# Performance work log

Measured on AMD Instinct MI355X. Metric: run time of the kernel, lower is better.

The kernel has to match this reference:

```python
import jax, jax.numpy as jnp
import numpy as np

DEPTH = 3

def _rx(theta):
    c, s = jnp.cos(theta / 2), jnp.sin(theta / 2)
    return jnp.stack([jnp.stack([c + 0j, -1j * s], -1),
                      jnp.stack([-1j * s, c + 0j], -1)], -2)

def _ry(theta):
    c, s = jnp.cos(theta / 2), jnp.sin(theta / 2)
    return jnp.stack([jnp.stack([c + 0j, -s + 0j], -1),
                      jnp.stack([s + 0j, c + 0j], -1)], -2)

def _rz(theta):
    e = jnp.exp(-0.5j * theta.astype(jnp.complex64))
    z = jnp.zeros_like(e)
    return jnp.stack([jnp.stack([e, z], -1),
                      jnp.stack([z, jnp.conj(e)], -1)], -2)

def _apply_1q(state, U, q):
    # state: (batch, 2,2,...,2); wire q lives on axis q+1. U: (2,2) or (batch,2,2)
    s = jnp.moveaxis(state, q + 1, -1)
    if U.ndim == 3:
        s = jnp.einsum('b...i,bji->b...j', s, U)
    else:
        s = jnp.einsum('...i,ji->...j', s, U)
    return jnp.moveaxis(s, -1, q + 1)

def _apply_cnot(state, c, t):
    s = jnp.moveaxis(state, (c + 1, t + 1), (-2, -1))
    s = jnp.concatenate([s[..., 0:1, :], s[..., 1:2, ::-1]], axis=-2)
    return jnp.moveaxis(s, (-2, -1), (c + 1, t + 1))

def _circuit(x, params):
    batch, n = x.shape
    depth = params.shape[0]
    state = jnp.zeros((batch,) + (2,) * n, jnp.complex64)
    state = state.at[(slice(None),) + (0,) * n].set(1.0)
    # data-encoding RX with per-sample angles
    for q in range(n):
        state = _apply_1q(state, _rx(x[:, q].astype(jnp.complex64).real), q)
    for l in range(depth):
        for q in range(n):
            state = _apply_1q(state, _rx(params[l, q, 0]), q)
            state = _apply_1q(state, _ry(params[l, q, 1]), q)
            state = _apply_1q(state, _rz(params[l, q, 2]), q)
        for q in range(n - 1):
            state = _apply_cnot(state, q, q + 1)
        state = _apply_cnot(state, n - 1, 0)
    probs = state.real ** 2 + state.imag ** 2  # (batch, 2,...,2)
    exps = []
    for w in range(n):
        p = jnp.moveaxis(probs, w + 1, 1).reshape(batch, 2, -1).sum(-1)
        exps.append(p[:, 0] - p[:, 1])  # <Z_w> = P(0) - P(1)
    return jnp.stack(exps, axis=1)


def setup_inputs() -> dict:
    key = jax.random.key(0)
    k1, k2 = jax.random.split(key)
    batch, n = 128, 14
    x = jax.random.normal(k1, (batch, n), dtype=jnp.float32)
    params = jax.random.normal(k2, (DEPTH, n, 3), dtype=jnp.float32)
    return {"x": x, "params": params}


def reference(x, params):
    return _circuit(x, params)
```

## Files before the change

kernel.cpp:

```cpp
#include <hip/hip_runtime.h>

namespace {

using v2f = __attribute__((ext_vector_type(2))) float;

constexpr int NQ      = 14;
constexpr int NSTATES = 1 << NQ;
constexpr int BLOCK   = 1024;
constexpr int NWAVES  = BLOCK / 64;

constexpr unsigned cparity(unsigned x){ x^=x>>8; x^=x>>4; x^=x>>2; x^=x>>1; return x&1u; }

struct Mat { unsigned row[NQ]; unsigned col[NQ]; };

constexpr Mat m_after(int nr){
  Mat m{};
  for(int p=0;p<NQ;++p){ m.row[p]=1u<<p; m.col[p]=1u<<p; }
  for(int l=0;l<nr;++l)
    for(int q=0;q<NQ;++q){
      int cq=(q==NQ-1)?NQ-1:q, tq=(q==NQ-1)?0:q+1;
      int Pc=NQ-1-cq, Pt=NQ-1-tq;
      m.row[Pt]^=m.row[Pc]; m.col[Pc]^=m.col[Pt];
    }
  return m;
}

constexpr Mat M1=m_after(1), M2=m_after(2), M3=m_after(3);
constexpr unsigned amask(int q){ return M1.col[NQ-1-q]; }
constexpr unsigned arow (int q){ return M1.row[NQ-1-q]; }
constexpr unsigned bmask(int q){ return M2.col[NQ-1-q]; }
constexpr unsigned brow (int q){ return M2.row[NQ-1-q]; }

constexpr int rank_of(const unsigned* v, int n){
  unsigned a[24]{};
  for(int i=0;i<n;++i) a[i]=v[i];
  int r=0;
  for(int bit=15;bit>=0;--bit){
    int p=-1;
    for(int i=r;i<n;++i){ if((a[i]>>bit)&1){ p=i; break; } }
    if(p<0) continue;
    unsigned t=a[r]; a[r]=a[p]; a[p]=t;
    for(int i=0;i<n;++i) if(i!=r && ((a[i]>>bit)&1)) a[i]^=a[r];
    ++r;
  }
  return r;
}

struct Plan {
  unsigned A[14], B[14], C[14];
  int BlaneGi[6]; unsigned BlanePi4[6];
  int BregGi[4];  unsigned BregEps[4];
  int CregGi[4];  unsigned CregEps[4];
  int ClaneGi[4]; unsigned ClaneEps[4];
  unsigned EJ4[14], ET[14];
};

constexpr Plan make_plan(){
  Plan P{};
  for(int t=0;t<14;++t) P.A[t]=amask(t);
  for(int t=0;t<4;++t){ P.B[t]=amask(10+t); P.BregGi[t]=10+t; }
  bool used[14]{}; int picked[14]{}; int np=0;
  {
    unsigned cur[20]{}; int nc=0;
    for(int t=0;t<4;++t) cur[nc++]=P.B[t];
    for(int q=0;q<14 && np<10;++q){
      cur[nc]=bmask(q);
      if(rank_of(cur,nc+1)==nc+1){ ++nc; picked[np++]=q; used[q]=true; }
    }
  }
  for(int i=0;i<6;++i){ P.B[4+i]=bmask(picked[i]); P.BlaneGi[i]=14+picked[i]; }
  int wq[4]{}, un[4]{}; int nu=0;
  for(int i=0;i<4;++i){ wq[i]=picked[6+i]; P.B[10+i]=bmask(wq[i]); P.CregGi[i]=14+wq[i]; }
  for(int q=0;q<14;++q) if(!used[q]) un[nu++]=q;
  for(int i=0;i<4;++i) P.ClaneGi[i]=14+un[i];
  for(int i=0;i<4;++i){ unsigned m=0;
    for(int t=0;t<10;++t) m |= cparity(arow(10+i)&P.B[4+t])<<t;
    P.BregEps[i]=m; }
  for(int i=0;i<6;++i){ unsigned m=0;
    for(int t=0;t<4;++t) m |= cparity(brow(picked[i])&P.B[t])<<t;
    P.BlanePi4[i]=m; }
  for(int t=0;t<4;++t) P.C[t]=bmask(wq[t]);
  for(int t=0;t<4;++t) P.C[4+t]=bmask(un[t]);
  {
    unsigned cc[20]{}; int n=0;
    for(int t=0;t<8;++t) cc[n++]=P.C[t];
    int pos=8;
    for(int p=0;p<14 && pos<14;++p){
      cc[n]=1u<<p;
      if(rank_of(cc,n+1)==n+1){ P.C[pos]=1u<<p; ++n; ++pos; }
    }
  }
  for(int i=0;i<4;++i){ unsigned m=0;
    for(int t=0;t<10;++t) m |= cparity(brow(wq[i])&P.C[4+t])<<t;
    P.CregEps[i]=m; }
  for(int i=0;i<4;++i){ unsigned m=0;
    for(int t=0;t<10;++t){ if(t==i) continue; m |= cparity(brow(un[i])&P.C[4+t])<<t; }
    P.ClaneEps[i]=m; }
  for(int w=0;w<14;++w){
    unsigned R=M3.row[NQ-1-w]; unsigned mj=0, mt=0;
    for(int t=0;t<4;++t)  mj |= cparity(R&P.C[t])<<t;
    for(int t=0;t<10;++t) mt |= cparity(R&P.C[4+t])<<t;
    P.EJ4[w]=mj; P.ET[w]=mt;
  }
  return P;
}

constexpr Plan PL = make_plan();
static_assert(rank_of(PL.A,14)==14, "phase A map not bijective");
static_assert(rank_of(PL.B,14)==14, "phase B map not bijective");
static_assert(rank_of(PL.C,14)==14, "phase C map not bijective");

struct Inv { unsigned col[NQ]; };
constexpr Inv inv_basis(const unsigned* bas){
  unsigned vec[NQ]{}, cmb[NQ]{}; bool used[NQ]{}; int pivk[NQ]{};
  for(int k=0;k<NQ;++k){ vec[k]=bas[k]; cmb[k]=1u<<k; }
  for(int b=0;b<NQ;++b){
    int p=-1;
    for(int k=0;k<NQ;++k) if(!used[k] && ((vec[k]>>b)&1)){ p=k; break; }
    used[p]=true; pivk[b]=p;
    for(int k=0;k<NQ;++k) if(k!=p && ((vec[k]>>b)&1)){ vec[k]^=vec[p]; cmb[k]^=cmb[p]; }
  }
  Inv R{};
  for(int b=0;b<NQ;++b) R.col[b]=cmb[pivk[b]];
  return R;
}
constexpr bool check_inv(const unsigned* bas, const Inv& iv){
  for(int p=0;p<NQ;++p){
    unsigned s=0;
    for(int k=0;k<NQ;++k) if((iv.col[p]>>k)&1) s^=bas[k];
    if(s != (1u<<p)) return false;
  }
  return true;
}
constexpr Inv IA = inv_basis(PL.A), IB = inv_basis(PL.B), IC = inv_basis(PL.C);
static_assert(check_inv(PL.A, IA), "IA");
static_assert(check_inv(PL.B, IB), "IB");
static_assert(check_inv(PL.C, IC), "IC");

struct Trans { unsigned t[NQ]; };
constexpr Trans trans_phys(const Inv& iv){
  Trans T{};
  for(int p=0;p<NQ;++p) T.t[p]=iv.col[p];
  return T;
}
constexpr Trans trans_of(const unsigned* cur, const Inv& iv){
  Trans T{};
  for(int k=0;k<NQ;++k){
    unsigned c=0;
    for(int p=0;p<NQ;++p) if((cur[k]>>p)&1) c^=iv.col[p];
    T.t[k]=c;
  }
  return T;
}
constexpr Trans T_PA = trans_phys(IA);
constexpr Trans T_AB = trans_of(PL.A, IB);
constexpr Trans T_BC = trans_of(PL.B, IC);

struct CJ { unsigned v[16]; };
constexpr CJ mk_cj(const Trans& T){
  CJ c{};
  for(int j=0;j<16;++j){
    unsigned s=0;
    for(int b=0;b<4;++b) if((j>>b)&1) s^=T.t[b];
    c.v[j]=s;
  }
  return c;
}
constexpr CJ CJ_PA=mk_cj(T_PA), CJ_AB=mk_cj(T_AB), CJ_BC=mk_cj(T_BC);

__device__ __forceinline__ v2f mkv(float a, float b){ v2f r; r[0]=a; r[1]=b; return r; }

__device__ __forceinline__ v2f pk_mul(v2f a, v2f b){
  v2f d; asm("v_pk_mul_f32 %0, %1, %2 op_sel:[0,0] op_sel_hi:[1,1]" : "=v"(d) : "v"(a), "v"(b)); return d;
}
__device__ __forceinline__ v2f pk_fma(v2f a, v2f b, v2f c){
  v2f d; asm("v_pk_fma_f32 %0, %1, %2, %3 op_sel:[0,0,0] op_sel_hi:[1,1,1]" : "=v"(d) : "v"(a), "v"(b), "v"(c)); return d;
}
__device__ __forceinline__ v2f pk_fma_swap1(v2f a, v2f b, v2f c){
  v2f d; asm("v_pk_fma_f32 %0, %1, %2, %3 op_sel:[0,1,0] op_sel_hi:[1,0,1]" : "=v"(d) : "v"(a), "v"(b), "v"(c)); return d;
}
__device__ __forceinline__ v2f cmul_pk(v2f uxx, v2f uyn, v2f s){ return pk_fma_swap1(uyn, s, pk_mul(uxx, s)); }
__device__ __forceinline__ v2f cfma_pk(v2f uxx, v2f uyn, v2f s, v2f acc){ return pk_fma_swap1(uyn, s, pk_fma(uxx, s, acc)); }

__device__ __forceinline__ float2 cmulf(float2 a, float2 b){
  return make_float2(a.x*b.x - a.y*b.y, a.x*b.y + a.y*b.x);
}
__device__ __forceinline__ v2f sel2(bool c, v2f x, v2f y){ v2f r; r[0]=c?x[0]:y[0]; r[1]=c?x[1]:y[1]; return r; }

struct GC { v2f u00x,u00n,u01x,u01n,u10x,u10n,u11x,u11n; };
__device__ __forceinline__ GC load_gc(const v2f* __restrict__ g){
  GC c{g[0],g[1],g[2],g[3],g[4],g[5],g[6],g[7]}; return c;
}

template<int CTRL>
__device__ __forceinline__ int dpp(int x){
  return __builtin_amdgcn_update_dpp(0, x, CTRL, 0xF, 0xF, true);
}
__device__ __forceinline__ int x32(int x, unsigned lane){
  auto r = __builtin_amdgcn_permlane32_swap((unsigned)x, (unsigned)x, false, false);
  return (lane & 32u) ? (int)r[0] : (int)r[1];
}
template<int K>
__device__ __forceinline__ v2f xpart(v2f v, unsigned lane){
  int x0=__float_as_int(v[0]), x1=__float_as_int(v[1]);
  int y0, y1;
  if constexpr (K==0){ y0=dpp<0xB1>(x0);  y1=dpp<0xB1>(x1); }
  else if constexpr (K==1){ y0=dpp<0x4E>(x0);  y1=dpp<0x4E>(x1); }
  else if constexpr (K==2){
    y0=__builtin_amdgcn_ds_swizzle(x0,0x101F);
    y1=__builtin_amdgcn_ds_swizzle(x1,0x101F);
  }
  else if constexpr (K==3){ y0=dpp<0x128>(x0); y1=dpp<0x128>(x1); }
  else if constexpr (K==4){
    y0=__builtin_amdgcn_ds_swizzle(x0,0x401F);
    y1=__builtin_amdgcn_ds_swizzle(x1,0x401F);
  }
  else { y0=x32(x0,lane); y1=x32(x1,lane); }
  v2f r; r[0]=__int_as_float(y0); r[1]=__int_as_float(y1); return r;
}

template<int BIT>
__device__ __forceinline__ void reg_gate(v2f (&a)[16], const GC& c, bool eps){
  v2f m00x=sel2(eps,c.u11x,c.u00x), m00n=sel2(eps,c.u11n,c.u00n);
  v2f m01x=sel2(eps,c.u10x,c.u01x), m01n=sel2(eps,c.u10n,c.u01n);
  v2f m10x=sel2(eps,c.u01x,c.u10x), m10n=sel2(eps,c.u01n,c.u10n);
  v2f m11x=sel2(eps,c.u00x,c.u11x), m11n=sel2(eps,c.u00n,c.u11n);
#pragma unroll
  for(int v=0; v<16; ++v){
    if(!((v>>BIT)&1)){
      int w = v | (1<<BIT);
      v2f a0=a[v], a1=a[w];
      a[v] = cfma_pk(m01x,m01n,a1, cmul_pk(m00x,m00n,a0));
      a[w] = cfma_pk(m11x,m11n,a1, cmul_pk(m10x,m10n,a0));
    }
  }
}

template<int XK, unsigned PI4>
__device__ __forceinline__ void lane_gate(v2f (&a)[16], const GC& c, bool sel, unsigned lane){
  v2f kax0=sel2(sel,c.u11x,c.u00x), kan0=sel2(sel,c.u11n,c.u00n);
  v2f kbx0=sel2(sel,c.u10x,c.u01x), kbn0=sel2(sel,c.u10n,c.u01n);
  v2f kax1=sel2(sel,c.u00x,c.u11x), kan1=sel2(sel,c.u00n,c.u11n);
  v2f kbx1=sel2(sel,c.u01x,c.u10x), kbn1=sel2(sel,c.u01n,c.u10n);
#pragma unroll
  for(int j=0;j<16;++j){
    v2f th = xpart<XK>(a[j], lane);
    bool pi = (__builtin_popcount(PI4 & (unsigned)j) & 1) != 0;
    v2f kax = pi?kax1:kax0, kan = pi?kan1:kan0;
    v2f kbx = pi?kbx1:kbx0, kbn = pi?kbn1:kbn0;
    a[j] = cfma_pk(kbx,kbn,th, cmul_pk(kax,kan,a[j]));
  }
}

__device__ __forceinline__ unsigned nb_of(unsigned tid, const unsigned (&t)[NQ]){
  unsigned s=0;
#pragma unroll
  for(int k=0;k<10;++k) s ^= t[4+k] & (0u-((tid>>k)&1u));
  return s;
}

__device__ __forceinline__ void scatter16(v2f* __restrict__ st, const v2f (&a)[16],
                                          unsigned nb, const CJ& cj){
#pragma unroll
  for(int j=0;j<16;++j){
    unsigned d = nb ^ cj.v[j];
    st[d + (d>>4)] = a[j];
  }
}

__global__ void prep_gates(const float* __restrict__ prm, float* __restrict__ wsf){
  int t = threadIdx.x;
  if(t >= 2*NQ) return;
  int l = 1 + t/NQ, q = t % NQ;
  float ax=prm[(l*NQ+q)*3+0], ay=prm[(l*NQ+q)*3+1], az=prm[(l*NQ+q)*3+2];
  float cx,sx,cy,sy,cz,sz;
  sincosf(0.5f*ax,&sx,&cx); sincosf(0.5f*ay,&sy,&cy); sincosf(0.5f*az,&sz,&cz);
  float2 M00=make_float2(cy*cx, sy*sx),  M01=make_float2(-sy*cx,-cy*sx);
  float2 M10=make_float2(sy*cx,-cy*sx),  M11=make_float2(cy*cx,-sy*sx);
  float2 ez =make_float2(cz,-sz), ezc=make_float2(cz,sz);
  float2 U00=cmulf(ez,M00), U01=cmulf(ez,M01), U10=cmulf(ezc,M10), U11=cmulf(ezc,M11);
  float* o = wsf + t*16;
  o[0]=U00.x; o[1]=U00.x; o[2]=-U00.y; o[3]=U00.y;
  o[4]=U01.x; o[5]=U01.x; o[6]=-U01.y; o[7]=U01.y;
  o[8]=U10.x; o[9]=U10.x; o[10]=-U10.y; o[11]=U10.y;
  o[12]=U11.x; o[13]=U11.x; o[14]=-U11.y; o[15]=U11.y;
}

__global__ __launch_bounds__(BLOCK, 4) void qsim_kernel(
    const float* __restrict__ x,
    const float* __restrict__ prm,
    const float* __restrict__ gw,
    float* __restrict__ out)
{
  __shared__ v2f    st[BLOCK*17];
  __shared__ v2f    Utab[28*8];
  __shared__ float2 l0c[NQ][2];
  __shared__ float  red[NWAVES][NQ];

  const int b = blockIdx.x;
  const unsigned tid = threadIdx.x;
  const unsigned lane = tid & 63u;

  if(tid < 28*16) ((float*)Utab)[tid] = gw[tid];
  if(tid < NQ){
    int q = tid;
    float ax = prm[q*3+0] + x[b*NQ+q];
    float ay = prm[q*3+1], az = prm[q*3+2];
    float cx,sx,cy,sy,cz,sz;
    sincosf(0.5f*ax,&sx,&cx); sincosf(0.5f*ay,&sy,&cy); sincosf(0.5f*az,&sz,&cz);
    l0c[q][0] = cmulf(make_float2(cz,-sz), make_float2(cy*cx,  sy*sx));
    l0c[q][1] = cmulf(make_float2(cz, sz), make_float2(sy*cx, -cy*sx));
  }
  __syncthreads();

  {
    float2 Pk = l0c[0][(tid>>9)&1];
#pragma unroll
    for(int q=1;q<10;++q) Pk = cmulf(Pk, l0c[q][(tid>>(9-q))&1]);
    float2 t2[2], t4[4];
    t2[0]=cmulf(Pk,l0c[10][0]); t2[1]=cmulf(Pk,l0c[10][1]);
#pragma unroll
    for(int i=0;i<2;++i){ t4[2*i]=cmulf(t2[i],l0c[11][0]); t4[2*i+1]=cmulf(t2[i],l0c[11][1]); }
    v2f a[16];
#pragma unroll
    for(int j=0;j<16;++j){
      float2 v = cmulf(cmulf(t4[j>>2], l0c[12][(j>>1)&1]), l0c[13][j&1]);
      a[j] = mkv(v.x, v.y);
    }
    scatter16(st, a, nb_of(tid, T_PA.t), CJ_PA);
  }
  __syncthreads();

  {
    v2f a[16];
    const int rb = (int)tid*17;
#pragma unroll
    for(int j=0;j<16;++j) a[j] = st[rb + j];
    reg_gate<0>(a, load_gc(Utab+0*8), false);
    reg_gate<1>(a, load_gc(Utab+1*8), false);
    reg_gate<2>(a, load_gc(Utab+2*8), false);
    reg_gate<3>(a, load_gc(Utab+3*8), false);
    lane_gate<0,0u>(a, load_gc(Utab+4*8), (tid&1)!=0,  lane);
    lane_gate<1,0u>(a, load_gc(Utab+5*8), (tid&2)!=0,  lane);
    lane_gate<2,0u>(a, load_gc(Utab+6*8), (tid&4)!=0,  lane);
    lane_gate<3,0u>(a, load_gc(Utab+7*8), (tid&8)!=0,  lane);
    lane_gate<4,0u>(a, load_gc(Utab+8*8), (tid&16)!=0, lane);
    lane_gate<5,0u>(a, load_gc(Utab+9*8), (tid&32)!=0, lane);
    __syncthreads();
    scatter16(st, a, nb_of(tid, T_AB.t), CJ_AB);
  }
  __syncthreads();

  {
    v2f a[16];
    const int rb = (int)tid*17;
#pragma unroll
    for(int j=0;j<16;++j) a[j] = st[rb + j];
    reg_gate<0>(a, load_gc(Utab+PL.BregGi[0]*8), (__builtin_popcount(PL.BregEps[0]&tid)&1)!=0);
    reg_gate<1>(a, load_gc(Utab+PL.BregGi[1]*8), (__builtin_popcount(PL.BregEps[1]&tid)&1)!=0);
    reg_gate<2>(a, load_gc(Utab+PL.BregGi[2]*8), (__builtin_popcount(PL.BregEps[2]&tid)&1)!=0);
    reg_gate<3>(a, load_gc(Utab+PL.BregGi[3]*8), (__builtin_popcount(PL.BregEps[3]&tid)&1)!=0);
    lane_gate<0,PL.BlanePi4[0]>(a, load_gc(Utab+PL.BlaneGi[0]*8), (tid&1)!=0,  lane);
    lane_gate<1,PL.BlanePi4[1]>(a, load_gc(Utab+PL.BlaneGi[1]*8), (tid&2)!=0,  lane);
    lane_gate<2,PL.BlanePi4[2]>(a, load_gc(Utab+PL.BlaneGi[2]*8), (tid&4)!=0,  lane);
    lane_gate<3,PL.BlanePi4[3]>(a, load_gc(Utab+PL.BlaneGi[3]*8), (tid&8)!=0,  lane);
    lane_gate<4,PL.BlanePi4[4]>(a, load_gc(Utab+PL.BlaneGi[4]*8), (tid&16)!=0, lane);
    lane_gate<5,PL.BlanePi4[5]>(a, load_gc(Utab+PL.BlaneGi[5]*8), (tid&32)!=0, lane);
    __syncthreads();
    scatter16(st, a, nb_of(tid, T_BC.t), CJ_BC);
  }
  __syncthreads();

  {
    v2f a[16];
    const int rb = (int)tid*17;
#pragma unroll
    for(int j=0;j<16;++j) a[j] = st[rb + j];
    reg_gate<0>(a, load_gc(Utab+PL.CregGi[0]*8), (__builtin_popcount(PL.CregEps[0]&tid)&1)!=0);
    reg_gate<1>(a, load_gc(Utab+PL.CregGi[1]*8), (__builtin_popcount(PL.CregEps[1]&tid)&1)!=0);
    reg_gate<2>(a, load_gc(Utab+PL.CregGi[2]*8), (__builtin_popcount(PL.CregEps[2]&tid)&1)!=0);
    reg_gate<3>(a, load_gc(Utab+PL.CregGi[3]*8), (__builtin_popcount(PL.CregEps[3]&tid)&1)!=0);
    lane_gate<0,0u>(a, load_gc(Utab+PL.ClaneGi[0]*8),
        (((tid&1u)!=0) != ((__builtin_popcount(PL.ClaneEps[0]&tid)&1)!=0)), lane);
    lane_gate<1,0u>(a, load_gc(Utab+PL.ClaneGi[1]*8),
        (((tid&2u)!=0) != ((__builtin_popcount(PL.ClaneEps[1]&tid)&1)!=0)), lane);
    lane_gate<2,0u>(a, load_gc(Utab+PL.ClaneGi[2]*8),
        (((tid&4u)!=0) != ((__builtin_popcount(PL.ClaneEps[2]&tid)&1)!=0)), lane);
    lane_gate<3,0u>(a, load_gc(Utab+PL.ClaneGi[3]*8),
        (((tid&8u)!=0) != ((__builtin_popcount(PL.ClaneEps[3]&tid)&1)!=0)), lane);

    float acc[NQ];
#pragma unroll
    for(int w=0;w<NQ;++w) acc[w]=0.f;
#pragma unroll
    for(int j=0;j<16;++j){
      float p = a[j][0]*a[j][0] + a[j][1]*a[j][1];
#pragma unroll
      for(int w=0;w<NQ;++w){
        if(__builtin_popcount(PL.EJ4[w] & (unsigned)j) & 1) acc[w]-=p; else acc[w]+=p;
      }
    }
    const int wave = tid >> 6;
#pragma unroll
    for(int w=0;w<NQ;++w){
      float v = (__builtin_popcount(PL.ET[w]&tid)&1) ? -acc[w] : acc[w];
#pragma unroll
      for(int off=32; off>0; off>>=1) v += __shfl_down(v, off, 64);
      if(lane==0) red[wave][w]=v;
    }
    __syncthreads();
    if(tid < NQ){
      float s=0.f;
#pragma unroll
      for(int wv=0; wv<NWAVES; ++wv) s += red[wv][tid];
      out[b*NQ + tid] = s;
    }
  }
}

}

extern "C" void kernel_launch(void* const* d_in, const int* in_sizes, int n_in,
                              void* d_out, int out_size, void* d_ws, size_t ws_size,
                              hipStream_t stream) {
  const float* x   = (const float*)d_in[0];
  const float* prm = (const float*)d_in[1];
  float* out = (float*)d_out;
  const int batch = in_sizes[0] / NQ;
  prep_gates<<<1, 64, 0, stream>>>(prm, (float*)d_ws);
  qsim_kernel<<<batch, BLOCK, 0, stream>>>(x, prm, (const float*)d_ws, out);
}
```

Before: 43.67 us.

## Fuse gate prep into main kernel, drop packed-FP asm, use Walsh-Hadamard reduction

After: 37.97 us. 13.1% less time.

```diff
diff --git a/kernel.cpp b/kernel.cpp
--- a/kernel.cpp
+++ b/kernel.cpp
@@ -1,8 +1,6 @@
 #include <hip/hip_runtime.h>
 
 namespace {
-
-using v2f = __attribute__((ext_vector_type(2))) float;
 
 constexpr int NQ      = 14;
 constexpr int NSTATES = 1 << NQ;
@@ -168,28 +166,26 @@
 }
 constexpr CJ CJ_PA=mk_cj(T_PA), CJ_AB=mk_cj(T_AB), CJ_BC=mk_cj(T_BC);
 
-__device__ __forceinline__ v2f mkv(float a, float b){ v2f r; r[0]=a; r[1]=b; return r; }
-
-__device__ __forceinline__ v2f pk_mul(v2f a, v2f b){
-  v2f d; asm("v_pk_mul_f32 %0, %1, %2 op_sel:[0,0] op_sel_hi:[1,1]" : "=v"(d) : "v"(a), "v"(b)); return d;
-}
-__device__ __forceinline__ v2f pk_fma(v2f a, v2f b, v2f c){
-  v2f d; asm("v_pk_fma_f32 %0, %1, %2, %3 op_sel:[0,0,0] op_sel_hi:[1,1,1]" : "=v"(d) : "v"(a), "v"(b), "v"(c)); return d;
-}
-__device__ __forceinline__ v2f pk_fma_swap1(v2f a, v2f b, v2f c){
-  v2f d; asm("v_pk_fma_f32 %0, %1, %2, %3 op_sel:[0,1,0] op_sel_hi:[1,0,1]" : "=v"(d) : "v"(a), "v"(b), "v"(c)); return d;
-}
-__device__ __forceinline__ v2f cmul_pk(v2f uxx, v2f uyn, v2f s){ return pk_fma_swap1(uyn, s, pk_mul(uxx, s)); }
-__device__ __forceinline__ v2f cfma_pk(v2f uxx, v2f uyn, v2f s, v2f acc){ return pk_fma_swap1(uyn, s, pk_fma(uxx, s, acc)); }
-
-__device__ __forceinline__ float2 cmulf(float2 a, float2 b){
-  return make_float2(a.x*b.x - a.y*b.y, a.x*b.y + a.y*b.x);
-}
-__device__ __forceinline__ v2f sel2(bool c, v2f x, v2f y){ v2f r; r[0]=c?x[0]:y[0]; r[1]=c?x[1]:y[1]; return r; }
-
-struct GC { v2f u00x,u00n,u01x,u01n,u10x,u10n,u11x,u11n; };
-__device__ __forceinline__ GC load_gc(const v2f* __restrict__ g){
-  GC c{g[0],g[1],g[2],g[3],g[4],g[5],g[6],g[7]}; return c;
+__device__ __forceinline__ float2 cmul2(float2 a, float2 b){
+  return make_float2(fmaf(a.x, b.x, -(a.y * b.y)),
+                     fmaf(a.x, b.y,  a.y * b.x));
+}
+__device__ __forceinline__ float2 cfma2(float2 a, float2 b, float2 c){
+  return make_float2(fmaf(a.x, b.x, fmaf(-a.y, b.y, c.x)),
+                     fmaf(a.x, b.y, fmaf( a.y, b.x, c.y)));
+}
+__device__ __forceinline__ float2 sel2f(bool c, float2 x, float2 y){
+  return make_float2(c ? x.x : y.x, c ? x.y : y.y);
+}
+
+struct GC { float2 u00,u01,u10,u11; };
+__device__ __forceinline__ GC load_gc(const float2* __restrict__ g){
+  const float4* p = reinterpret_cast<const float4*>(g);
+  float4 q0=p[0], q1=p[1];
+  GC c;
+  c.u00=make_float2(q0.x,q0.y); c.u01=make_float2(q0.z,q0.w);
+  c.u10=make_float2(q1.x,q1.y); c.u11=make_float2(q1.z,q1.w);
+  return c;
 }
 
 template<int CTRL>
@@ -201,8 +197,8 @@
   return (lane & 32u) ? (int)r[0] : (int)r[1];
 }
 template<int K>
-__device__ __forceinline__ v2f xpart(v2f v, unsigned lane){
-  int x0=__float_as_int(v[0]), x1=__float_as_int(v[1]);
+__device__ __forceinline__ float2 xpart(float2 v, unsigned lane){
+  int x0=__float_as_int(v.x), x1=__float_as_int(v.y);
   int y0, y1;
   if constexpr (K==0){ y0=dpp<0xB1>(x0);  y1=dpp<0xB1>(x1); }
   else if constexpr (K==1){ y0=dpp<0x4E>(x0);  y1=dpp<0x4E>(x1); }
@@ -216,39 +212,36 @@
     y1=__builtin_amdgcn_ds_swizzle(x1,0x401F);
   }
   else { y0=x32(x0,lane); y1=x32(x1,lane); }
-  v2f r; r[0]=__int_as_float(y0); r[1]=__int_as_float(y1); return r;
+  return make_float2(__int_as_float(y0), __int_as_float(y1));
 }
 
 template<int BIT>
-__device__ __forceinline__ void reg_gate(v2f (&a)[16], const GC& c, bool eps){
-  v2f m00x=sel2(eps,c.u11x,c.u00x), m00n=sel2(eps,c.u11n,c.u00n);
-  v2f m01x=sel2(eps,c.u10x,c.u01x), m01n=sel2(eps,c.u10n,c.u01n);
-  v2f m10x=sel2(eps,c.u01x,c.u10x), m10n=sel2(eps,c.u01n,c.u10n);
-  v2f m11x=sel2(eps,c.u00x,c.u11x), m11n=sel2(eps,c.u00n,c.u11n);
+__device__ __forceinline__ void reg_gate(float2 (&a)[16], const GC& c, bool eps){
+  float2 m00=sel2f(eps,c.u11,c.u00), m01=sel2f(eps,c.u10,c.u01);
+  float2 m10=sel2f(eps,c.u01,c.u10), m11=sel2f(eps,c.u00,c.u11);
 #pragma unroll
   for(int v=0; v<16; ++v){
     if(!((v>>BIT)&1)){
       int w = v | (1<<BIT);
-      v2f a0=a[v], a1=a[w];
-      a[v] = cfma_pk(m01x,m01n,a1, cmul_pk(m00x,m00n,a0));
-      a[w] = cfma_pk(m11x,m11n,a1, cmul_pk(m10x,m10n,a0));
+      float2 a0=a[v], a1=a[w];
+      a[v] = cfma2(m01, a1, cmul2(m00, a0));
+      a[w] = cfma2(m11, a1, cmul2(m10, a0));
     }
   }
 }
 
 template<int XK, unsigned PI4>
-__device__ __forceinline__ void lane_gate(v2f (&a)[16], const GC& c, bool sel, unsigned lane){
-  v2f kax0=sel2(sel,c.u11x,c.u00x), kan0=sel2(sel,c.u11n,c.u00n);
-  v2f kbx0=sel2(sel,c.u10x,c.u01x), kbn0=sel2(sel,c.u10n,c.u01n);
-  v2f kax1=sel2(sel,c.u00x,c.u11x), kan1=sel2(sel,c.u00n,c.u11n);
-  v2f kbx1=sel2(sel,c.u01x,c.u10x), kbn1=sel2(sel,c.u01n,c.u10n);
+__device__ __forceinline__ void lane_gate(float2 (&a)[16], const GC& c, bool sel, unsigned lane){
+  float2 ka0=sel2f(sel,c.u11,c.u00), kb0=sel2f(sel,c.u10,c.u01);
+  float2 ka1=sel2f(sel,c.u00,c.u11), kb1=sel2f(sel,c.u01,c.u10);
+  float2 th[16];
+#pragma unroll
+  for(int j=0;j<16;++j) th[j] = xpart<XK>(a[j], lane);
 #pragma unroll
   for(int j=0;j<16;++j){
-    v2f th = xpart<XK>(a[j], lane);
     bool pi = (__builtin_popcount(PI4 & (unsigned)j) & 1) != 0;
-    v2f kax = pi?kax1:kax0, kan = pi?kan1:kan0;
-    v2f kbx = pi?kbx1:kbx0, kbn = pi?kbn1:kbn0;
-    a[j] = cfma_pk(kbx,kbn,th, cmul_pk(kax,kan,a[j]));
+    float2 ka = pi?ka1:ka0, kb = pi?kb1:kb0;
+    a[j] = cfma2(kb, th[j], cmul2(ka, a[j]));
   }
 }
 
@@ -259,7 +252,7 @@
   return s;
 }
 
-__device__ __forceinline__ void scatter16(v2f* __restrict__ st, const v2f (&a)[16],
+__device__ __forceinline__ void scatter16(float2* __restrict__ st, const float2 (&a)[16],
                                           unsigned nb, const CJ& cj){
 #pragma unroll
   for(int j=0;j<16;++j){
@@ -268,32 +261,13 @@
   }
 }
 
-__global__ void prep_gates(const float* __restrict__ prm, float* __restrict__ wsf){
-  int t = threadIdx.x;
-  if(t >= 2*NQ) return;
-  int l = 1 + t/NQ, q = t % NQ;
-  float ax=prm[(l*NQ+q)*3+0], ay=prm[(l*NQ+q)*3+1], az=prm[(l*NQ+q)*3+2];
-  float cx,sx,cy,sy,cz,sz;
-  sincosf(0.5f*ax,&sx,&cx); sincosf(0.5f*ay,&sy,&cy); sincosf(0.5f*az,&sz,&cz);
-  float2 M00=make_float2(cy*cx, sy*sx),  M01=make_float2(-sy*cx,-cy*sx);
-  float2 M10=make_float2(sy*cx,-cy*sx),  M11=make_float2(cy*cx,-sy*sx);
-  float2 ez =make_float2(cz,-sz), ezc=make_float2(cz,sz);
-  float2 U00=cmulf(ez,M00), U01=cmulf(ez,M01), U10=cmulf(ezc,M10), U11=cmulf(ezc,M11);
-  float* o = wsf + t*16;
-  o[0]=U00.x; o[1]=U00.x; o[2]=-U00.y; o[3]=U00.y;
-  o[4]=U01.x; o[5]=U01.x; o[6]=-U01.y; o[7]=U01.y;
-  o[8]=U10.x; o[9]=U10.x; o[10]=-U10.y; o[11]=U10.y;
-  o[12]=U11.x; o[13]=U11.x; o[14]=-U11.y; o[15]=U11.y;
-}
-
 __global__ __launch_bounds__(BLOCK, 4) void qsim_kernel(
     const float* __restrict__ x,
     const float* __restrict__ prm,
-    const float* __restrict__ gw,
     float* __restrict__ out)
 {
-  __shared__ v2f    st[BLOCK*17];
-  __shared__ v2f    Utab[28*8];
+  __shared__ float2 st[BLOCK*17];
+  __shared__ alignas(16) float2 Utab[28*4];
   __shared__ float2 l0c[NQ][2];
   __shared__ float  red[NWAVES][NQ];
 
@@ -301,109 +275,126 @@
   const unsigned tid = threadIdx.x;
   const unsigned lane = tid & 63u;
 
-  if(tid < 28*16) ((float*)Utab)[tid] = gw[tid];
+  if(tid < 28){
+    int t = tid;
+    int l = 1 + t/NQ, q = t % NQ;
+    float ax=prm[(l*NQ+q)*3+0], ay=prm[(l*NQ+q)*3+1], az=prm[(l*NQ+q)*3+2];
+    float cx,sx,cy,sy,cz,sz;
+    sincosf(0.5f*ax,&sx,&cx); sincosf(0.5f*ay,&sy,&cy); sincosf(0.5f*az,&sz,&cz);
+    float2 M00=make_float2(cy*cx, sy*sx),  M01=make_float2(-sy*cx,-cy*sx);
+    float2 M10=make_float2(sy*cx,-cy*sx),  M11=make_float2(cy*cx,-sy*sx);
+    float2 ez =make_float2(cz,-sz), ezc=make_float2(cz,sz);
+    float2* U = &Utab[t*4];
+    U[0]=cmul2(ez,M00); U[1]=cmul2(ez,M01);
+    U[2]=cmul2(ezc,M10); U[3]=cmul2(ezc,M11);
+  }
   if(tid < NQ){
     int q = tid;
     float ax = prm[q*3+0] + x[b*NQ+q];
     float ay = prm[q*3+1], az = prm[q*3+2];
     float cx,sx,cy,sy,cz,sz;
     sincosf(0.5f*ax,&sx,&cx); sincosf(0.5f*ay,&sy,&cy); sincosf(0.5f*az,&sz,&cz);
-    l0c[q][0] = cmulf(make_float2(cz,-sz), make_float2(cy*cx,  sy*sx));
-    l0c[q][1] = cmulf(make_float2(cz, sz), make_float2(sy*cx, -cy*sx));
+    l0c[q][0] = cmul2(make_float2(cz,-sz), make_float2(cy*cx,  sy*sx));
+    l0c[q][1] = cmul2(make_float2(cz, sz), make_float2(sy*cx, -cy*sx));
   }
   __syncthreads();
 
   {
-    float2 Pk = l0c[0][(tid>>9)&1];
-#pragma unroll
-    for(int q=1;q<10;++q) Pk = cmulf(Pk, l0c[q][(tid>>(9-q))&1]);
+    float2 p01 = cmul2(l0c[0][(tid>>9)&1],  l0c[1][(tid>>8)&1]);
+    float2 p23 = cmul2(l0c[2][(tid>>7)&1],  l0c[3][(tid>>6)&1]);
+    float2 p45 = cmul2(l0c[4][(tid>>5)&1],  l0c[5][(tid>>4)&1]);
+    float2 p67 = cmul2(l0c[6][(tid>>3)&1],  l0c[7][(tid>>2)&1]);
+    float2 p89 = cmul2(l0c[8][(tid>>1)&1],  l0c[9][tid&1]);
+    float2 Pk  = cmul2(cmul2(cmul2(p01,p23), cmul2(p45,p67)), p89);
     float2 t2[2], t4[4];
-    t2[0]=cmulf(Pk,l0c[10][0]); t2[1]=cmulf(Pk,l0c[10][1]);
-#pragma unroll
-    for(int i=0;i<2;++i){ t4[2*i]=cmulf(t2[i],l0c[11][0]); t4[2*i+1]=cmulf(t2[i],l0c[11][1]); }
-    v2f a[16];
+    t2[0]=cmul2(Pk,l0c[10][0]); t2[1]=cmul2(Pk,l0c[10][1]);
+#pragma unroll
+    for(int i=0;i<2;++i){ t4[2*i]=cmul2(t2[i],l0c[11][0]); t4[2*i+1]=cmul2(t2[i],l0c[11][1]); }
+    float2 a[16];
 #pragma unroll
     for(int j=0;j<16;++j){
-      float2 v = cmulf(cmulf(t4[j>>2], l0c[12][(j>>1)&1]), l0c[13][j&1]);
-      a[j] = mkv(v.x, v.y);
+      a[j] = cmul2(cmul2(t4[j>>2], l0c[12][(j>>1)&1]), l0c[13][j&1]);
     }
     scatter16(st, a, nb_of(tid, T_PA.t), CJ_PA);
   }
   __syncthreads();
 
   {
-    v2f a[16];
+    float2 a[16];
     const int rb = (int)tid*17;
 #pragma unroll
     for(int j=0;j<16;++j) a[j] = st[rb + j];
-    reg_gate<0>(a, load_gc(Utab+0*8), false);
-    reg_gate<1>(a, load_gc(Utab+1*8), false);
-    reg_gate<2>(a, load_gc(Utab+2*8), false);
-    reg_gate<3>(a, load_gc(Utab+3*8), false);
-    lane_gate<0,0u>(a, load_gc(Utab+4*8), (tid&1)!=0,  lane);
-    lane_gate<1,0u>(a, load_gc(Utab+5*8), (tid&2)!=0,  lane);
-    lane_gate<2,0u>(a, load_gc(Utab+6*8), (tid&4)!=0,  lane);
-    lane_gate<3,0u>(a, load_gc(Utab+7*8), (tid&8)!=0,  lane);
-    lane_gate<4,0u>(a, load_gc(Utab+8*8), (tid&16)!=0, lane);
-    lane_gate<5,0u>(a, load_gc(Utab+9*8), (tid&32)!=0, lane);
+    reg_gate<0>(a, load_gc(Utab+0*4), false);
+    reg_gate<1>(a, load_gc(Utab+1*4), false);
+    reg_gate<2>(a, load_gc(Utab+2*4), false);
+    reg_gate<3>(a, load_gc(Utab+3*4), false);
+    lane_gate<0,0u>(a, load_gc(Utab+4*4), (tid&1)!=0,  lane);
+    lane_gate<1,0u>(a, load_gc(Utab+5*4), (tid&2)!=0,  lane);
+    lane_gate<2,0u>(a, load_gc(Utab+6*4), (tid&4)!=0,  lane);
+    lane_gate<3,0u>(a, load_gc(Utab+7*4), (tid&8)!=0,  lane);
+    lane_gate<4,0u>(a, load_gc(Utab+8*4), (tid&16)!=0, lane);
+    lane_gate<5,0u>(a, load_gc(Utab+9*4), (tid&32)!=0, lane);
     __syncthreads();
     scatter16(st, a, nb_of(tid, T_AB.t), CJ_AB);
   }
   __syncthreads();
 
   {
-    v2f a[16];
+    float2 a[16];
     const int rb = (int)tid*17;
 #pragma unroll
     for(int j=0;j<16;++j) a[j] = st[rb + j];
-    reg_gate<0>(a, load_gc(Utab+PL.BregGi[0]*8), (__builtin_popcount(PL.BregEps[0]&tid)&1)!=0);
-    reg_gate<1>(a, load_gc(Utab+PL.BregGi[1]*8), (__builtin_popcount(PL.BregEps[1]&tid)&1)!=0);
-    reg_gate<2>(a, load_gc(Utab+PL.BregGi[2]*8), (__builtin_popcount(PL.BregEps[2]&tid)&1)!=0);
-    reg_gate<3>(a, load_gc(Utab+PL.BregGi[3]*8), (__builtin_popcount(PL.BregEps[3]&tid)&1)!=0);
-    lane_gate<0,PL.BlanePi4[0]>(a, load_gc(Utab+PL.BlaneGi[0]*8), (tid&1)!=0,  lane);
-    lane_gate<1,PL.BlanePi4[1]>(a, load_gc(Utab+PL.BlaneGi[1]*8), (tid&2)!=0,  lane);
-    lane_gate<2,PL.BlanePi4[2]>(a, load_gc(Utab+PL.BlaneGi[2]*8), (tid&4)!=0,  lane);
-    lane_gate<3,PL.BlanePi4[3]>(a, load_gc(Utab+PL.BlaneGi[3]*8), (tid&8)!=0,  lane);
-    lane_gate<4,PL.BlanePi4[4]>(a, load_gc(Utab+PL.BlaneGi[4]*8), (tid&16)!=0, lane);
-    lane_gate<5,PL.BlanePi4[5]>(a, load_gc(Utab+PL.BlaneGi[5]*8), (tid&32)!=0, lane);
+    reg_gate<0>(a, load_gc(Utab+PL.BregGi[0]*4), (__builtin_popcount(PL.BregEps[0]&tid)&1)!=0);
+    reg_gate<1>(a, load_gc(Utab+PL.BregGi[1]*4), (__builtin_popcount(PL.BregEps[1]&tid)&1)!=0);
+    reg_gate<2>(a, load_gc(Utab+PL.BregGi[2]*4), (__builtin_popcount(PL.BregEps[2]&tid)&1)!=0);
+    reg_gate<3>(a, load_gc(Utab+PL.BregGi[3]*4), (__builtin_popcount(PL.BregEps[3]&tid)&1)!=0);
+    lane_gate<0,PL.BlanePi4[0]>(a, load_gc(Utab+PL.BlaneGi[0]*4), (tid&1)!=0,  lane);
+    lane_gate<1,PL.BlanePi4[1]>(a, load_gc(Utab+PL.BlaneGi[1]*4), (tid&2)!=0,  lane);
+    lane_gate<2,PL.BlanePi4[2]>(a, load_gc(Utab+PL.BlaneGi[2]*4), (tid&4)!=0,  lane);
+    lane_gate<3,PL.BlanePi4[3]>(a, load_gc(Utab+PL.BlaneGi[3]*4), (tid&8)!=0,  lane);
+    lane_gate<4,PL.BlanePi4[4]>(a, load_gc(Utab+PL.BlaneGi[4]*4), (tid&16)!=0, lane);
+    lane_gate<5,PL.BlanePi4[5]>(a, load_gc(Utab+PL.BlaneGi[5]*4), (tid&32)!=0, lane);
     __syncthreads();
     scatter16(st, a, nb_of(tid, T_BC.t), CJ_BC);
   }
   __syncthreads();
 
   {
-    v2f a[16];
+    float2 a[16];
     const int rb = (int)tid*17;
 #pragma unroll
     for(int j=0;j<16;++j) a[j] = st[rb + j];
-    reg_gate<0>(a, load_gc(Utab+PL.CregGi[0]*8), (__builtin_popcount(PL.CregEps[0]&tid)&1)!=0);
-    reg_gate<1>(a, load_gc(Utab+PL.CregGi[1]*8), (__builtin_popcount(PL.CregEps[1]&tid)&1)!=0);
-    reg_gate<2>(a, load_gc(Utab+PL.CregGi[2]*8), (__builtin_popcount(PL.CregEps[2]&tid)&1)!=0);
-    reg_gate<3>(a, load_gc(Utab+PL.CregGi[3]*8), (__builtin_popcount(PL.CregEps[3]&tid)&1)!=0);
-    lane_gate<0,0u>(a, load_gc(Utab+PL.ClaneGi[0]*8),
+    reg_gate<0>(a, load_gc(Utab+PL.CregGi[0]*4), (__builtin_popcount(PL.CregEps[0]&tid)&1)!=0);
+    reg_gate<1>(a, load_gc(Utab+PL.CregGi[1]*4), (__builtin_popcount(PL.CregEps[1]&tid)&1)!=0);
+    reg_gate<2>(a, load_gc(Utab+PL.CregGi[2]*4), (__builtin_popcount(PL.CregEps[2]&tid)&1)!=0);
+    reg_gate<3>(a, load_gc(Utab+PL.CregGi[3]*4), (__builtin_popcount(PL.CregEps[3]&tid)&1)!=0);
+    lane_gate<0,0u>(a, load_gc(Utab+PL.ClaneGi[0]*4),
         (((tid&1u)!=0) != ((__builtin_popcount(PL.ClaneEps[0]&tid)&1)!=0)), lane);
-    lane_gate<1,0u>(a, load_gc(Utab+PL.ClaneGi[1]*8),
+    lane_gate<1,0u>(a, load_gc(Utab+PL.ClaneGi[1]*4),
         (((tid&2u)!=0) != ((__builtin_popcount(PL.ClaneEps[1]&tid)&1)!=0)), lane);
-    lane_gate<2,0u>(a, load_gc(Utab+PL.ClaneGi[2]*8),
+    lane_gate<2,0u>(a, load_gc(Utab+PL.ClaneGi[2]*4),
         (((tid&4u)!=0) != ((__builtin_popcount(PL.ClaneEps[2]&tid)&1)!=0)), lane);
-    lane_gate<3,0u>(a, load_gc(Utab+PL.ClaneGi[3]*8),
+    lane_gate<3,0u>(a, load_gc(Utab+PL.ClaneGi[3]*4),
         (((tid&8u)!=0) != ((__builtin_popcount(PL.ClaneEps[3]&tid)&1)!=0)), lane);
 
-    float acc[NQ];
-#pragma unroll
-    for(int w=0;w<NQ;++w) acc[w]=0.f;
-#pragma unroll
-    for(int j=0;j<16;++j){
-      float p = a[j][0]*a[j][0] + a[j][1]*a[j][1];
-#pragma unroll
-      for(int w=0;w<NQ;++w){
-        if(__builtin_popcount(PL.EJ4[w] & (unsigned)j) & 1) acc[w]-=p; else acc[w]+=p;
+    float p[16];
+#pragma unroll
+    for(int j=0;j<16;++j) p[j] = a[j].x*a[j].x + a[j].y*a[j].y;
+#pragma unroll
+    for(int bstep=1; bstep<16; bstep<<=1){
+#pragma unroll
+      for(int j=0;j<16;++j){
+        if(!(j & bstep)){
+          float u = p[j], v = p[j|bstep];
+          p[j] = u + v;
+          p[j|bstep] = u - v;
+        }
       }
     }
     const int wave = tid >> 6;
 #pragma unroll
     for(int w=0;w<NQ;++w){
-      float v = (__builtin_popcount(PL.ET[w]&tid)&1) ? -acc[w] : acc[w];
+      float v = (__builtin_popcount(PL.ET[w]&tid)&1) ? -p[PL.EJ4[w]] : p[PL.EJ4[w]];
 #pragma unroll
       for(int off=32; off>0; off>>=1) v += __shfl_down(v, off, 64);
       if(lane==0) red[wave][w]=v;
@@ -427,6 +418,5 @@
   const float* prm = (const float*)d_in[1];
   float* out = (float*)d_out;
   const int batch = in_sizes[0] / NQ;
-  prep_gates<<<1, 64, 0, stream>>>(prm, (float*)d_ws);
-  qsim_kernel<<<batch, BLOCK, 0, stream>>>(x, prm, (const float*)d_ws, out);
-}
+  qsim_kernel<<<batch, BLOCK, 0, stream>>>(x, prm, out);
+}
```
